# Kernel optimization log

Hardware: AMD Instinct MI355X
Metric: run time of the kernel (lower is better)

Reference implementation:

```python
import jax, jax.numpy as jnp
import numpy as np

N_NODES = 50000
N_EDGES = 800000
HIDDEN = 128


def setup_inputs() -> dict:
    key = jax.random.key(0)
    ks = jax.random.split(key, 8)
    z = jax.random.normal(ks[0], (N_NODES, HIDDEN), dtype=jnp.float32)
    weights = jax.random.normal(ks[1], (N_EDGES, 1), dtype=jnp.float32)
    sources = jax.random.randint(ks[2], (N_EDGES,), 0, N_NODES)
    dests = jax.random.randint(ks[3], (N_EDGES,), 0, N_NODES)
    # Linear params (stored [in, out]); scale ~ 1/sqrt(fan_in) like torch default
    in_m = 2 * HIDDEN + 1
    in_u = 2 * HIDDEN
    Wm = jax.random.uniform(ks[4], (in_m, HIDDEN), dtype=jnp.float32, minval=-1.0, maxval=1.0) / np.sqrt(in_m)
    bm = jax.random.uniform(ks[5], (HIDDEN,), dtype=jnp.float32, minval=-1.0, maxval=1.0) / np.sqrt(in_m)
    Wu = jax.random.uniform(ks[6], (in_u, HIDDEN), dtype=jnp.float32, minval=-1.0, maxval=1.0) / np.sqrt(in_u)
    bu = jax.random.uniform(ks[7], (HIDDEN,), dtype=jnp.float32, minval=-1.0, maxval=1.0) / np.sqrt(in_u)
    return {"z": z, "weights": weights, "sources": sources, "dests": dests,
            "Wm": Wm, "bm": bm, "Wu": Wu, "bu": bu}


def reference(z, weights, sources, dests, Wm, bm, Wu, bu):
    n = z.shape[0]
    # gather + concat message input: [E, 2d+1]
    inp = jnp.concatenate([z[dests], z[sources], weights], axis=1)
    messages = inp @ Wm + bm                      # [E, d]
    # scatter_reduce amax over destination nodes; empty segments -> -inf
    m = jax.ops.segment_max(messages, dests, num_segments=n)
    m = jnp.where(jnp.isneginf(m), jnp.zeros_like(m), m)
    h = jnp.concatenate([z, m], axis=1) @ Wu + bu  # [N, d]
    return h
```

## Files before the change

### kernel.cpp

```cpp
#include <hip/hip_runtime.h>
#include <math.h>

#define HIDDEN 128
#define PAD_DEG 64
#define NPART 8
#define CHUNK 4096
#define CNT_STRIDE 16

typedef __attribute__((ext_vector_type(8))) _Float16 f16x8;
typedef __attribute__((ext_vector_type(4))) float f32x4;
typedef __attribute__((ext_vector_type(2))) _Float16 h2;

__device__ inline unsigned short f2h(float x) {
    _Float16 h = (_Float16)x;
    return __builtin_bit_cast(unsigned short, h);
}
__device__ inline float h2f(unsigned short u) {
    return (float)__builtin_bit_cast(_Float16, u);
}
__device__ inline float h2f_lo(unsigned int u) { return h2f((unsigned short)(u & 0xffff)); }
__device__ inline float h2f_hi(unsigned int u) { return h2f((unsigned short)(u >> 16)); }
__device__ inline h2 hmax2(h2 a, h2 b) {
    h2 r;
    r[0] = a[0] > b[0] ? a[0] : b[0];
    r[1] = a[1] > b[1] ? a[1] : b[1];
    return r;
}

__global__ void prep_kernel(const float* __restrict__ Wm, const float* __restrict__ Wu,
                            unsigned short* __restrict__ WmT0, unsigned short* __restrict__ WmT1,
                            unsigned short* __restrict__ WuT, float* __restrict__ wlast,
                            int* __restrict__ counts, int n) {
    int t = blockIdx.x * blockDim.x + threadIdx.x;
    if (t < 16384) {
        int nn = t >> 7, k = t & 127;
        WmT0[t] = f2h(Wm[k * 128 + nn]);
    } else if (t < 32768) {
        int s = t - 16384;
        int nn = s >> 7, k = s & 127;
        WmT1[s] = f2h(Wm[(128 + k) * 128 + nn]);
    } else if (t < 65536) {
        int s = t - 32768;
        int nn = s >> 8, k = s & 255;
        WuT[s] = f2h(Wu[k * 128 + nn]);
    } else if (t < 65664) {
        int i = t - 65536;
        wlast[i] = Wm[256 * 128 + i];
    } else if (t < 65664 + 4 * n) {
        ((int4*)counts)[t - 65664] = make_int4(0, 0, 0, 0);
    }
}

__global__ __launch_bounds__(256) void fused_sg(const int* __restrict__ dests,
                                                const int* __restrict__ sources,
                                                const float* __restrict__ weights,
                                                int* __restrict__ counts,
                                                unsigned int* __restrict__ edge_pk,
                                                int E, int span, int n,
                                                const float* __restrict__ Z,
                                                const unsigned short* __restrict__ WmT0,
                                                const unsigned short* __restrict__ WmT1,
                                                unsigned short* __restrict__ P1h,
                                                unsigned short* __restrict__ P2h,
                                                int nscatter) {
    __shared__ unsigned short As[64][136];
    __shared__ unsigned short Bs[128][136];

    if (blockIdx.x < nscatter) {
        const int part = blockIdx.x & (NPART - 1);
        const int chunk = blockIdx.x >> 3;
        const int lo = part * span;
        const int hi = min(lo + span, n);
        const int base = chunk * CHUNK + threadIdx.x * 4;

        int dd[16];
        unsigned int pk[16];
        int pos[16];

#pragma unroll
        for (int g = 0; g < 4; ++g) {
            int e = base + g * 1024;
            if (e + 3 < E) {
                int4 dq = *(const int4*)&dests[e];
                int4 sq = *(const int4*)&sources[e];
                float4 wq = *(const float4*)&weights[e];
                dd[g * 4 + 0] = dq.x; dd[g * 4 + 1] = dq.y;
                dd[g * 4 + 2] = dq.z; dd[g * 4 + 3] = dq.w;
                pk[g * 4 + 0] = (unsigned int)(sq.x & 0xffff) | ((unsigned int)f2h(wq.x) << 16);
                pk[g * 4 + 1] = (unsigned int)(sq.y & 0xffff) | ((unsigned int)f2h(wq.y) << 16);
                pk[g * 4 + 2] = (unsigned int)(sq.z & 0xffff) | ((unsigned int)f2h(wq.z) << 16);
                pk[g * 4 + 3] = (unsigned int)(sq.w & 0xffff) | ((unsigned int)f2h(wq.w) << 16);
            } else {
#pragma unroll
                for (int j = 0; j < 4; ++j) {
                    int ej = e + j;
                    if (ej < E) {
                        dd[g * 4 + j] = dests[ej];
                        pk[g * 4 + j] = (unsigned int)(sources[ej] & 0xffff) |
                                        ((unsigned int)f2h(weights[ej]) << 16);
                    } else {
                        dd[g * 4 + j] = -1;
                        pk[g * 4 + j] = 0;
                    }
                }
            }
        }

#pragma unroll
        for (int k = 0; k < 16; ++k) {
            bool act = (dd[k] >= lo) && (dd[k] < hi);
            pos[k] = act ? atomicAdd(&counts[(size_t)dd[k] * CNT_STRIDE], 1) : PAD_DEG;
        }

#pragma unroll
        for (int k = 0; k < 16; ++k) {
            if (pos[k] < PAD_DEG) {
                edge_pk[(size_t)dd[k] * PAD_DEG + pos[k]] = pk[k];
            }
        }
        return;
    }

    const int m0 = (blockIdx.x - nscatter) * 64;
    const int tid = threadIdx.x;
    const int wave = tid >> 6, lane = tid & 63;
    const int l15 = lane & 15, q = lane >> 4;
    const int wrow = wave * 16;

#pragma unroll
    for (int i = 0; i < 4; ++i) {
        int f = tid + i * 256;
        int row = f >> 4, c8 = f & 15;
        int gr = min(m0 + row, n - 1);
        const float4* src = (const float4*)&Z[(size_t)gr * 128 + c8 * 8];
        float4 a = src[0], b = src[1];
        f16x8 hv;
        hv[0] = (_Float16)a.x; hv[1] = (_Float16)a.y; hv[2] = (_Float16)a.z; hv[3] = (_Float16)a.w;
        hv[4] = (_Float16)b.x; hv[5] = (_Float16)b.y; hv[6] = (_Float16)b.z; hv[7] = (_Float16)b.w;
        *(f16x8*)&As[row][c8 * 8] = hv;
    }

    for (int part = 0; part < 2; ++part) {
        const float4* bsrc = (const float4*)(part == 0 ? WmT0 : WmT1);
        unsigned short* Out = part == 0 ? P1h : P2h;

#pragma unroll
        for (int i = 0; i < 8; ++i) {
            int f = tid + i * 256;
            int row = f >> 4, c4 = f & 15;
            *(float4*)&Bs[row][c4 * 8] = bsrc[row * 16 + c4];
        }
        __syncthreads();

        f32x4 acc[8];
#pragma unroll
        for (int nt = 0; nt < 8; ++nt) acc[nt] = (f32x4){0.f, 0.f, 0.f, 0.f};

#pragma unroll
        for (int ks = 0; ks < 4; ++ks) {
            int k0 = ks * 32;
            f16x8 a = *(const f16x8*)&As[wrow + l15][k0 + q * 8];
#pragma unroll
            for (int nt = 0; nt < 8; ++nt) {
                f16x8 b = *(const f16x8*)&Bs[nt * 16 + l15][k0 + q * 8];
                acc[nt] = __builtin_amdgcn_mfma_f32_16x16x32_f16(a, b, acc[nt], 0, 0, 0);
            }
        }

#pragma unroll
        for (int nt = 0; nt < 8; ++nt) {
#pragma unroll
            for (int r = 0; r < 4; ++r) {
                int row = m0 + wrow + q * 4 + r;
                if (row < n) Out[(size_t)row * 128 + nt * 16 + l15] = f2h(acc[nt][r]);
            }
        }
        __syncthreads();
    }
}

__global__ __launch_bounds__(256) void segmax_kernel(const unsigned short* __restrict__ P1h,
                                                     const unsigned short* __restrict__ P2h,
                                                     const int* __restrict__ counts,
                                                     const unsigned int* __restrict__ edge_pk,
                                                     const float* __restrict__ wlast,
                                                     const float* __restrict__ bm,
                                                     unsigned short* __restrict__ Mh, int n) {
    const int wave = threadIdx.x >> 6;
    const int lane = threadIdx.x & 63;
    const int v = blockIdx.x * 4 + wave;
    if (v >= n) return;

    const int l16 = lane & 15;
    const int e4 = lane >> 4;
    const uint4* P2q = (const uint4*)P2h;
    const int cnt = min(counts[(size_t)v * CNT_STRIDE], PAD_DEG);

    int pk = (lane < cnt) ? (int)edge_pk[(size_t)v * PAD_DEG + lane] : 0;

    float4 wfa = ((const float4*)wlast)[l16 * 2];
    float4 wfb = ((const float4*)wlast)[l16 * 2 + 1];
    h2 wl0, wl1, wl2, wl3;
    wl0[0] = (_Float16)wfa.x; wl0[1] = (_Float16)wfa.y;
    wl1[0] = (_Float16)wfa.z; wl1[1] = (_Float16)wfa.w;
    wl2[0] = (_Float16)wfb.x; wl2[1] = (_Float16)wfb.y;
    wl3[0] = (_Float16)wfb.z; wl3[1] = (_Float16)wfb.w;

    const h2 NEGINF = __builtin_bit_cast(h2, 0xFC00FC00u);
    h2 a0 = NEGINF, a1 = NEGINF, a2 = NEGINF, a3 = NEGINF;

    int j = 0;
    for (; j + 8 <= cnt; j += 8) {
        unsigned int pa = (unsigned int)__shfl(pk, j + e4);
        unsigned int pb = (unsigned int)__shfl(pk, j + 4 + e4);
        int sa = pa & 0xffff, sb = pb & 0xffff;
        uint4 ua = P2q[(size_t)sa * 16 + l16];
        uint4 ub = P2q[(size_t)sb * 16 + l16];
        h2 wva = __builtin_bit_cast(h2, (pa & 0xffff0000u) | (pa >> 16));
        h2 wvb = __builtin_bit_cast(h2, (pb & 0xffff0000u) | (pb >> 16));
        a0 = hmax2(a0, wva * wl0 + __builtin_bit_cast(h2, ua.x));
        a1 = hmax2(a1, wva * wl1 + __builtin_bit_cast(h2, ua.y));
        a2 = hmax2(a2, wva * wl2 + __builtin_bit_cast(h2, ua.z));
        a3 = hmax2(a3, wva * wl3 + __builtin_bit_cast(h2, ua.w));
        a0 = hmax2(a0, wvb * wl0 + __builtin_bit_cast(h2, ub.x));
        a1 = hmax2(a1, wvb * wl1 + __builtin_bit_cast(h2, ub.y));
        a2 = hmax2(a2, wvb * wl2 + __builtin_bit_cast(h2, ub.z));
        a3 = hmax2(a3, wvb * wl3 + __builtin_bit_cast(h2, ub.w));
    }
    for (; j < cnt; j += 4) {
        int idx = j + e4;
        bool valid = idx < cnt;
        unsigned int pa = (unsigned int)__shfl(pk, valid ? idx : 0);
        if (valid) {
            int sa = pa & 0xffff;
            uint4 ua = P2q[(size_t)sa * 16 + l16];
            h2 wva = __builtin_bit_cast(h2, (pa & 0xffff0000u) | (pa >> 16));
            a0 = hmax2(a0, wva * wl0 + __builtin_bit_cast(h2, ua.x));
            a1 = hmax2(a1, wva * wl1 + __builtin_bit_cast(h2, ua.y));
            a2 = hmax2(a2, wva * wl2 + __builtin_bit_cast(h2, ua.z));
            a3 = hmax2(a3, wva * wl3 + __builtin_bit_cast(h2, ua.w));
        }
    }

    a0 = hmax2(a0, __builtin_bit_cast(h2, __shfl_xor(__builtin_bit_cast(int, a0), 16)));
    a1 = hmax2(a1, __builtin_bit_cast(h2, __shfl_xor(__builtin_bit_cast(int, a1), 16)));
    a2 = hmax2(a2, __builtin_bit_cast(h2, __shfl_xor(__builtin_bit_cast(int, a2), 16)));
    a3 = hmax2(a3, __builtin_bit_cast(h2, __shfl_xor(__builtin_bit_cast(int, a3), 16)));
    a0 = hmax2(a0, __builtin_bit_cast(h2, __shfl_xor(__builtin_bit_cast(int, a0), 32)));
    a1 = hmax2(a1, __builtin_bit_cast(h2, __shfl_xor(__builtin_bit_cast(int, a1), 32)));
    a2 = hmax2(a2, __builtin_bit_cast(h2, __shfl_xor(__builtin_bit_cast(int, a2), 32)));
    a3 = hmax2(a3, __builtin_bit_cast(h2, __shfl_xor(__builtin_bit_cast(int, a3), 32)));

    if (e4 == 0) {
        uint4 o = make_uint4(0, 0, 0, 0);
        if (cnt > 0) {
            uint4 p1 = ((const uint4*)P1h)[(size_t)v * 16 + l16];
            float4 b0 = ((const float4*)bm)[l16 * 2];
            float4 b1 = ((const float4*)bm)[l16 * 2 + 1];
            float m0 = h2f_lo(p1.x) + b0.x + (float)a0[0];
            float m1 = h2f_hi(p1.x) + b0.y + (float)a0[1];
            float m2 = h2f_lo(p1.y) + b0.z + (float)a1[0];
            float m3 = h2f_hi(p1.y) + b0.w + (float)a1[1];
            float m4 = h2f_lo(p1.z) + b1.x + (float)a2[0];
            float m5 = h2f_hi(p1.z) + b1.y + (float)a2[1];
            float m6 = h2f_lo(p1.w) + b1.z + (float)a3[0];
            float m7 = h2f_hi(p1.w) + b1.w + (float)a3[1];
            o.x = (unsigned int)f2h(m0) | ((unsigned int)f2h(m1) << 16);
            o.y = (unsigned int)f2h(m2) | ((unsigned int)f2h(m3) << 16);
            o.z = (unsigned int)f2h(m4) | ((unsigned int)f2h(m5) << 16);
            o.w = (unsigned int)f2h(m6) | ((unsigned int)f2h(m7) << 16);
        } else {
            unsigned int zh = (unsigned int)f2h(0.f);
            unsigned int zz = zh | (zh << 16);
            o = make_uint4(zz, zz, zz, zz);
        }
        ((uint4*)Mh)[(size_t)v * 16 + l16] = o;
    }
}

__global__ __launch_bounds__(256) void gemm_out(const float* __restrict__ Z,
                                                const unsigned short* __restrict__ Mh,
                                                const unsigned short* __restrict__ WuT,
                                                const float* __restrict__ bu,
                                                float* __restrict__ H, int n) {
    __shared__ unsigned short As[64][136];
    __shared__ unsigned short Bs[128][136];

    const int m0 = blockIdx.x * 64;
    const int tid = threadIdx.x;
    const int wave = tid >> 6, lane = tid & 63;
    const int l15 = lane & 15, q = lane >> 4;
    const int wrow = wave * 16;

    f32x4 acc[8];
#pragma unroll
    for (int nt = 0; nt < 8; ++nt) acc[nt] = (f32x4){0.f, 0.f, 0.f, 0.f};

    for (int h = 0; h < 2; ++h) {
#pragma unroll
        for (int i = 0; i < 8; ++i) {
            int f = tid + i * 256;
            int row = f >> 4, c4 = f & 15;
            *(float4*)&Bs[row][c4 * 8] = ((const float4*)WuT)[row * 32 + h * 16 + c4];
        }
        if (h == 0) {
#pragma unroll
            for (int i = 0; i < 4; ++i) {
                int f = tid + i * 256;
                int row = f >> 4, c8 = f & 15;
                int gr = min(m0 + row, n - 1);
                const float4* src = (const float4*)&Z[(size_t)gr * 128 + c8 * 8];
                float4 a = src[0], b = src[1];
                f16x8 hv;
                hv[0] = (_Float16)a.x; hv[1] = (_Float16)a.y; hv[2] = (_Float16)a.z; hv[3] = (_Float16)a.w;
                hv[4] = (_Float16)b.x; hv[5] = (_Float16)b.y; hv[6] = (_Float16)b.z; hv[7] = (_Float16)b.w;
                *(f16x8*)&As[row][c8 * 8] = hv;
            }
        } else {
#pragma unroll
            for (int i = 0; i < 4; ++i) {
                int f = tid + i * 256;
                int row = f >> 4, c4 = f & 15;
                int gr = min(m0 + row, n - 1);
                *(float4*)&As[row][c4 * 8] = ((const float4*)&Mh[(size_t)gr * 128])[c4];
            }
        }
        __syncthreads();

#pragma unroll
        for (int ks = 0; ks < 4; ++ks) {
            int k0 = ks * 32;
            f16x8 a = *(const f16x8*)&As[wrow + l15][k0 + q * 8];
#pragma unroll
            for (int nt = 0; nt < 8; ++nt) {
                f16x8 b = *(const f16x8*)&Bs[nt * 16 + l15][k0 + q * 8];
                acc[nt] = __builtin_amdgcn_mfma_f32_16x16x32_f16(a, b, acc[nt], 0, 0, 0);
            }
        }
        __syncthreads();
    }

#pragma unroll
    for (int nt = 0; nt < 8; ++nt) {
        int col = nt * 16 + l15;
        float bias = bu[col];
#pragma unroll
        for (int r = 0; r < 4; ++r) {
            int row = m0 + wrow + q * 4 + r;
            if (row < n) H[(size_t)row * 128 + col] = acc[nt][r] + bias;
        }
    }
}

extern "C" void kernel_launch(void* const* d_in, const int* in_sizes, int n_in,
                              void* d_out, int out_size, void* d_ws, size_t ws_size,
                              hipStream_t stream) {
    const float* z = (const float*)d_in[0];
    const float* weights = (const float*)d_in[1];
    const int* sources = (const int*)d_in[2];
    const int* dests = (const int*)d_in[3];
    const float* Wm = (const float*)d_in[4];
    const float* bm = (const float*)d_in[5];
    const float* Wu = (const float*)d_in[6];
    const float* bu = (const float*)d_in[7];

    const int n = in_sizes[0] / HIDDEN;
    const int E = in_sizes[1];
    float* H = (float*)d_out;

    char* w = (char*)d_ws;
    auto alloc = [&](size_t bytes) { void* p = w; w += (bytes + 255) & ~(size_t)255; return p; };
    unsigned short* P1h = (unsigned short*)alloc((size_t)n * 128 * 2);
    unsigned short* Mh  = (unsigned short*)alloc((size_t)n * 128 * 2);
    unsigned short* WmT0 = (unsigned short*)alloc(16384 * 2);
    unsigned short* WmT1 = (unsigned short*)alloc(16384 * 2);
    unsigned short* WuT  = (unsigned short*)alloc(32768 * 2);
    float* wlast = (float*)alloc(128 * 4);
    int* counts  = (int*)alloc((size_t)n * CNT_STRIDE * 4);
    unsigned int* edge_pk = (unsigned int*)alloc((size_t)n * PAD_DEG * 4);

    unsigned short* P2h = (unsigned short*)d_out;

    const int mblocks = (n + 63) / 64;
    const int prep_threads = 65664 + 4 * n;
    const int span = (n + NPART - 1) / NPART;
    const int nchunks = (E + CHUNK - 1) / CHUNK;
    const int nscatter = nchunks * NPART;

    prep_kernel<<<(prep_threads + 255) / 256, 256, 0, stream>>>(Wm, Wu, WmT0, WmT1, WuT,
                                                                wlast, counts, n);
    fused_sg<<<nscatter + mblocks, 256, 0, stream>>>(dests, sources, weights, counts,
                                                     edge_pk, E, span, n,
                                                     z, WmT0, WmT1, P1h, P2h, nscatter);
    segmax_kernel<<<(n + 3) / 4, 256, 0, stream>>>(P1h, P2h, counts, edge_pk,
                                                   wlast, bm, Mh, n);
    gemm_out<<<mblocks, 256, 0, stream>>>(z, Mh, WuT, bu, H, n);
}
```

Baseline: 191.0 us.

## Assign scatter destination partitions by hardware XCD with per-XCD atomic chunk queues

Scatter blocks now read their XCC id from a hardware register and take the destination partition matching that XCD, then pull edge chunks from a per-XCD atomic work counter until all chunks are done. The intent is to keep each partition's count atomics and edge writes inside one XCD's L2, so the count atomics can be workgroup-scope and cross-die coherence traffic is avoided. The scatter grid becomes a fixed 1024 persistent blocks. Correctness relies on every XCD getting at least one scatter block and on relaxed workgroup-scope atomics being coherent enough when blocks of the same XCD sit on different CUs, which is risky; if dispatch does not cover all XCDs, some partitions are never filled.

```diff
diff --git a/kernel.cpp b/kernel.cpp
--- a/kernel.cpp
+++ b/kernel.cpp
@@ -6,6 +6,8 @@
 #define NPART 8
 #define CHUNK 4096
 #define CNT_STRIDE 16
+#define NSCATTER_BLOCKS 1024
+#define XCC_GETREG_IMM 63508
 
 typedef __attribute__((ext_vector_type(8))) _Float16 f16x8;
 typedef __attribute__((ext_vector_type(4))) float f32x4;
@@ -30,7 +32,7 @@
 __global__ void prep_kernel(const float* __restrict__ Wm, const float* __restrict__ Wu,
                             unsigned short* __restrict__ WmT0, unsigned short* __restrict__ WmT1,
                             unsigned short* __restrict__ WuT, float* __restrict__ wlast,
-                            int* __restrict__ counts, int n) {
+                            int* __restrict__ counts, int* __restrict__ tick, int n) {
     int t = blockIdx.x * blockDim.x + threadIdx.x;
     if (t < 16384) {
         int nn = t >> 7, k = t & 127;
@@ -48,6 +50,8 @@
         wlast[i] = Wm[256 * 128 + i];
     } else if (t < 65664 + 4 * n) {
         ((int4*)counts)[t - 65664] = make_int4(0, 0, 0, 0);
+    } else if (t < 65664 + 4 * n + 128) {
+        tick[t - 65664 - 4 * n] = 0;
     }
 }
 
@@ -55,8 +59,9 @@
                                                 const int* __restrict__ sources,
                                                 const float* __restrict__ weights,
                                                 int* __restrict__ counts,
+                                                int* __restrict__ tick,
                                                 unsigned int* __restrict__ edge_pk,
-                                                int E, int span, int n,
+                                                int E, int span, int n, int nchunks,
                                                 const float* __restrict__ Z,
                                                 const unsigned short* __restrict__ WmT0,
                                                 const unsigned short* __restrict__ WmT1,
@@ -65,57 +70,71 @@
                                                 int nscatter) {
     __shared__ unsigned short As[64][136];
     __shared__ unsigned short Bs[128][136];
+    __shared__ int s_chunk;
 
     if (blockIdx.x < nscatter) {
-        const int part = blockIdx.x & (NPART - 1);
-        const int chunk = blockIdx.x >> 3;
-        const int lo = part * span;
+        const int xcd = (int)(__builtin_amdgcn_s_getreg(XCC_GETREG_IMM) & 7);
+        const int lo = xcd * span;
         const int hi = min(lo + span, n);
-        const int base = chunk * CHUNK + threadIdx.x * 4;
-
-        int dd[16];
-        unsigned int pk[16];
-        int pos[16];
-
-#pragma unroll
-        for (int g = 0; g < 4; ++g) {
-            int e = base + g * 1024;
-            if (e + 3 < E) {
-                int4 dq = *(const int4*)&dests[e];
-                int4 sq = *(const int4*)&sources[e];
-                float4 wq = *(const float4*)&weights[e];
-                dd[g * 4 + 0] = dq.x; dd[g * 4 + 1] = dq.y;
-                dd[g * 4 + 2] = dq.z; dd[g * 4 + 3] = dq.w;
-                pk[g * 4 + 0] = (unsigned int)(sq.x & 0xffff) | ((unsigned int)f2h(wq.x) << 16);
-                pk[g * 4 + 1] = (unsigned int)(sq.y & 0xffff) | ((unsigned int)f2h(wq.y) << 16);
-                pk[g * 4 + 2] = (unsigned int)(sq.z & 0xffff) | ((unsigned int)f2h(wq.z) << 16);
-                pk[g * 4 + 3] = (unsigned int)(sq.w & 0xffff) | ((unsigned int)f2h(wq.w) << 16);
-            } else {
-#pragma unroll
-                for (int j = 0; j < 4; ++j) {
-                    int ej = e + j;
-                    if (ej < E) {
-                        dd[g * 4 + j] = dests[ej];
-                        pk[g * 4 + j] = (unsigned int)(sources[ej] & 0xffff) |
-                                        ((unsigned int)f2h(weights[ej]) << 16);
-                    } else {
-                        dd[g * 4 + j] = -1;
-                        pk[g * 4 + j] = 0;
+
+        for (int it = 0; it <= nchunks; ++it) {
+            if (threadIdx.x == 0) {
+                s_chunk = __hip_atomic_fetch_add(&tick[xcd * 16], 1,
+                                                 __ATOMIC_RELAXED, __HIP_MEMORY_SCOPE_AGENT);
+            }
+            __syncthreads();
+            const int chunk = s_chunk;
+            __syncthreads();
+            if (chunk >= nchunks || chunk < 0) break;
+
+            const int base = chunk * CHUNK + threadIdx.x * 4;
+            int dd[16];
+            unsigned int pk[16];
+            int pos[16];
+
+#pragma unroll
+            for (int g = 0; g < 4; ++g) {
+                int e = base + g * 1024;
+                if (e + 3 < E) {
+                    int4 dq = *(const int4*)&dests[e];
+                    int4 sq = *(const int4*)&sources[e];
+                    float4 wq = *(const float4*)&weights[e];
+                    dd[g * 4 + 0] = dq.x; dd[g * 4 + 1] = dq.y;
+                    dd[g * 4 + 2] = dq.z; dd[g * 4 + 3] = dq.w;
+                    pk[g * 4 + 0] = (unsigned int)(sq.x & 0xffff) | ((unsigned int)f2h(wq.x) << 16);
+                    pk[g * 4 + 1] = (unsigned int)(sq.y & 0xffff) | ((unsigned int)f2h(wq.y) << 16);
+                    pk[g * 4 + 2] = (unsigned int)(sq.z & 0xffff) | ((unsigned int)f2h(wq.z) << 16);
+                    pk[g * 4 + 3] = (unsigned int)(sq.w & 0xffff) | ((unsigned int)f2h(wq.w) << 16);
+                } else {
+#pragma unroll
+                    for (int j = 0; j < 4; ++j) {
+                        int ej = e + j;
+                        if (ej < E) {
+                            dd[g * 4 + j] = dests[ej];
+                            pk[g * 4 + j] = (unsigned int)(sources[ej] & 0xffff) |
+                                            ((unsigned int)f2h(weights[ej]) << 16);
+                        } else {
+                            dd[g * 4 + j] = -1;
+                            pk[g * 4 + j] = 0;
+                        }
                     }
                 }
             }
-        }
-
-#pragma unroll
-        for (int k = 0; k < 16; ++k) {
-            bool act = (dd[k] >= lo) && (dd[k] < hi);
-            pos[k] = act ? atomicAdd(&counts[(size_t)dd[k] * CNT_STRIDE], 1) : PAD_DEG;
-        }
-
-#pragma unroll
-        for (int k = 0; k < 16; ++k) {
-            if (pos[k] < PAD_DEG) {
-                edge_pk[(size_t)dd[k] * PAD_DEG + pos[k]] = pk[k];
+
+#pragma unroll
+            for (int k = 0; k < 16; ++k) {
+                bool act = (dd[k] >= lo) && (dd[k] < hi);
+                pos[k] = act ? __hip_atomic_fetch_add(&counts[(size_t)dd[k] * CNT_STRIDE], 1,
+                                                      __ATOMIC_RELAXED,
+                                                      __HIP_MEMORY_SCOPE_WORKGROUP)
+                             : PAD_DEG;
+            }
+
+#pragma unroll
+            for (int k = 0; k < 16; ++k) {
+                if (pos[k] < PAD_DEG) {
+                    edge_pk[(size_t)dd[k] * PAD_DEG + pos[k]] = pk[k];
+                }
             }
         }
         return;
@@ -377,20 +396,21 @@
     unsigned short* WuT  = (unsigned short*)alloc(32768 * 2);
     float* wlast = (float*)alloc(128 * 4);
     int* counts  = (int*)alloc((size_t)n * CNT_STRIDE * 4);
+    int* tick    = (int*)alloc(128 * 4);
     unsigned int* edge_pk = (unsigned int*)alloc((size_t)n * PAD_DEG * 4);
 
     unsigned short* P2h = (unsigned short*)d_out;
 
     const int mblocks = (n + 63) / 64;
-    const int prep_threads = 65664 + 4 * n;
+    const int prep_threads = 65664 + 4 * n + 128;
     const int span = (n + NPART - 1) / NPART;
     const int nchunks = (E + CHUNK - 1) / CHUNK;
-    const int nscatter = nchunks * NPART;
+    const int nscatter = NSCATTER_BLOCKS;
 
     prep_kernel<<<(prep_threads + 255) / 256, 256, 0, stream>>>(Wm, Wu, WmT0, WmT1, WuT,
-                                                                wlast, counts, n);
-    fused_sg<<<nscatter + mblocks, 256, 0, stream>>>(dests, sources, weights, counts,
-                                                     edge_pk, E, span, n,
+                                                                wlast, counts, tick, n);
+    fused_sg<<<nscatter + mblocks, 256, 0, stream>>>(dests, sources, weights, counts, tick,
+                                                     edge_pk, E, span, n, nchunks,
                                                      z, WmT0, WmT1, P1h, P2h, nscatter);
     segmax_kernel<<<(n + 3) / 4, 256, 0, stream>>>(P1h, P2h, counts, edge_pk,
                                                    wlast, bm, Mh, n);
```

After: 193.6 us. No clear change (+1.4%).
